# Performance work log

Hardware: AMD Instinct MI355X
Metric: run time of the kernel (lower is better)

The kernel has to match this reference:

```python
import jax, jax.numpy as jnp
import numpy as np

USER_NUM = 1_000_000
ITEM_NUM = 100_000
N_FEATS = 8
DICT_SIZE = 10_000
VEC_DIM = 16
K = 32
BATCH = 16_384
TOTAL_DIM = (2 + N_FEATS) * VEC_DIM  # 160


def setup_inputs() -> dict:
    key = jax.random.key(0)
    ks = jax.random.split(key, 7)
    inputs = jax.random.randint(ks[0], (BATCH, 2 + N_FEATS), 0, DICT_SIZE, dtype=jnp.int32)
    user_table = jax.random.normal(ks[1], (USER_NUM, VEC_DIM), dtype=jnp.float32) * 0.05
    item_table = jax.random.normal(ks[2], (ITEM_NUM, VEC_DIM), dtype=jnp.float32) * 0.05
    feat_tables = jax.random.normal(ks[3], (N_FEATS, DICT_SIZE, VEC_DIM), dtype=jnp.float32) * 0.05
    w = jax.random.normal(ks[4], (TOTAL_DIM, 1), dtype=jnp.float32) * 0.05
    b = jnp.zeros((1,), dtype=jnp.float32)
    k_mat = jax.random.normal(ks[5], (TOTAL_DIM, K), dtype=jnp.float32) * (1.0 / np.sqrt(TOTAL_DIM))
    return {"inputs": inputs, "user_table": user_table, "item_table": item_table,
            "feat_tables": feat_tables, "w": w, "b": b, "k_mat": k_mat}


def reference(inputs, user_table, item_table, feat_tables, w, b, k_mat):
    B = inputs.shape[0]
    user_vec = user_table[inputs[:, 0]]            # [B, D]
    item_vec = item_table[inputs[:, 1]]            # [B, D]
    # gather each feature table with its own id column: [F, B, D]
    feat_vecs = jax.vmap(lambda tbl, idx: tbl[idx], in_axes=(0, 1))(feat_tables, inputs[:, 2:])
    feat_flat = jnp.transpose(feat_vecs, (1, 0, 2)).reshape(B, -1)  # [B, F*D]
    x = jnp.concatenate([user_vec, item_vec, feat_flat], axis=1)    # [B, total_dim]
    linear = x @ w + b                                              # [B, 1]
    inter_1 = jnp.square(x @ k_mat)                                 # [B, K]
    inter_2 = jnp.square(x) @ jnp.square(k_mat)                     # [B, K]
    cross = 0.5 * jnp.sum(inter_1 - inter_2, axis=1, keepdims=True) # [B, 1]
    return jax.nn.sigmoid(linear + cross)
```

## Files before the change

kernel.cpp:

```cpp
#include <hip/hip_runtime.h>
#include <hip/hip_bf16.h>
#include <math.h>

#define NFEAT 10
#define DICT 10000

typedef __attribute__((ext_vector_type(8))) short bf16x8;
typedef __attribute__((ext_vector_type(4))) float f32x4;
typedef __attribute__((ext_vector_type(4))) unsigned u32x4;

__device__ inline unsigned short f2bf(float f) {
    __hip_bfloat16 h = __float2bfloat16(f);
    unsigned short s;
    __builtin_memcpy(&s, &h, sizeof(s));
    return s;
}
__device__ inline unsigned cvt2(float lo, float hi) {
    return (unsigned)f2bf(lo) | ((unsigned)f2bf(hi) << 16);
}

__global__ __launch_bounds__(256, 2) void fm_fused(
    const int* __restrict__ inputs,
    const float* __restrict__ user_table,
    const float* __restrict__ item_table,
    const float* __restrict__ feat_tables,
    const float* __restrict__ wvec,
    const float* __restrict__ bb,
    const float* __restrict__ k_mat,
    float* __restrict__ out)
{
    __shared__ float part_t[2][16];

    const int tid   = threadIdx.x;
    const int lane  = tid & 63;
    const int wid   = tid >> 6;
    const int tile  = wid >> 1;
    const bool sq   = (wid & 1) != 0;
    const int gtile = blockIdx.x * 2 + tile;
    const int col   = lane & 15;
    const int kg    = lane >> 4;
    const int e     = gtile * 16 + col;
    const int fsel  = kg >> 1;
    const int hoff  = (kg & 1) * 8;

    int idx[5];
    #pragma unroll
    for (int c = 0; c < 5; ++c)
        idx[c] = inputs[e * NFEAT + 2 * c + fsel];

    float4 u0[5], u1[5];
    #pragma unroll
    for (int c = 0; c < 5; ++c) {
        const float* tbl = (c == 0)
            ? (fsel ? item_table : user_table)
            : (feat_tables + (size_t)(2 * c + fsel - 2) * (DICT * 16));
        const float* src = tbl + (size_t)idx[c] * 16 + hoff;
        u0[c] = *(const float4*)src;
        u1[c] = *(const float4*)(src + 4);
    }

    bf16x8 b0[5], b1[5];
    #pragma unroll
    for (int c = 0; c < 5; ++c) {
        const int dbase = c * 32 + kg * 8;
        float f0[8], f1[8];
        #pragma unroll
        for (int j = 0; j < 8; ++j) {
            f0[j] = k_mat[(dbase + j) * 32 + col];
            f1[j] = k_mat[(dbase + j) * 32 + 16 + col];
        }
        if (sq) {
            #pragma unroll
            for (int j = 0; j < 8; ++j) { f0[j] *= f0[j]; f1[j] *= f1[j]; }
        }
        u32x4 p0, p1;
        #pragma unroll
        for (int j = 0; j < 4; ++j) {
            p0[j] = cvt2(f0[2*j], f0[2*j+1]);
            p1[j] = cvt2(f1[2*j], f1[2*j+1]);
        }
        b0[c] = __builtin_bit_cast(bf16x8, p0);
        b1[c] = __builtin_bit_cast(bf16x8, p1);
    }

    f32x4 acc0 = {0,0,0,0};
    f32x4 acc1 = {0,0,0,0};
    #pragma unroll
    for (int c = 0; c < 5; ++c) {
        float4 v0 = u0[c], v1 = u1[c];
        if (sq) {
            v0.x *= v0.x; v0.y *= v0.y; v0.z *= v0.z; v0.w *= v0.w;
            v1.x *= v1.x; v1.y *= v1.y; v1.z *= v1.z; v1.w *= v1.w;
        }
        u32x4 p;
        p[0] = cvt2(v0.x, v0.y); p[1] = cvt2(v0.z, v0.w);
        p[2] = cvt2(v1.x, v1.y); p[3] = cvt2(v1.z, v1.w);
        bf16x8 a = __builtin_bit_cast(bf16x8, p);
        acc0 = __builtin_amdgcn_mfma_f32_16x16x32_bf16(a, b0[c], acc0, 0, 0, 0);
        acc1 = __builtin_amdgcn_mfma_f32_16x16x32_bf16(a, b1[c], acc1, 0, 0, 0);
    }

    float lin = 0.f;
    if (!sq) {
        #pragma unroll
        for (int c = 0; c < 5; ++c) {
            const int dbase = c * 32 + kg * 8;
            float4 w0 = *(const float4*)&wvec[dbase];
            float4 w1 = *(const float4*)&wvec[dbase + 4];
            lin = fmaf(u0[c].x, w0.x, lin); lin = fmaf(u0[c].y, w0.y, lin);
            lin = fmaf(u0[c].z, w0.z, lin); lin = fmaf(u0[c].w, w0.w, lin);
            lin = fmaf(u1[c].x, w1.x, lin); lin = fmaf(u1[c].y, w1.y, lin);
            lin = fmaf(u1[c].z, w1.z, lin); lin = fmaf(u1[c].w, w1.w, lin);
        }
        lin += __shfl_xor(lin, 16, 64);
        lin += __shfl_xor(lin, 32, 64);
    }

    float sv[4];
    #pragma unroll
    for (int r = 0; r < 4; ++r) {
        float v = sq ? (acc0[r] + acc1[r])
                     : (acc0[r]*acc0[r] + acc1[r]*acc1[r]);
        #pragma unroll
        for (int m = 1; m <= 8; m <<= 1)
            v += __shfl_xor(v, m, 64);
        sv[r] = v;
        if (sq && col == 0) part_t[tile][kg * 4 + r] = v;
    }
    __syncthreads();

    if (!sq) {
        const float bval = bb[0];
        #pragma unroll
        for (int r = 0; r < 4; ++r) {
            float lm = __shfl(lin, kg * 4 + r, 64);
            if (col == 0) {
                float z = lm + bval + 0.5f * (sv[r] - part_t[tile][kg * 4 + r]);
                out[gtile * 16 + kg * 4 + r] = 1.0f / (1.0f + __expf(-z));
            }
        }
    }
}

extern "C" void kernel_launch(void* const* d_in, const int* in_sizes, int n_in,
                              void* d_out, int out_size, void* d_ws, size_t ws_size,
                              hipStream_t stream) {
    const int*   inputs      = (const int*)  d_in[0];
    const float* user_table  = (const float*)d_in[1];
    const float* item_table  = (const float*)d_in[2];
    const float* feat_tables = (const float*)d_in[3];
    const float* w           = (const float*)d_in[4];
    const float* b           = (const float*)d_in[5];
    const float* k_mat       = (const float*)d_in[6];
    float* out = (float*)d_out;

    int nblocks = out_size / 32;
    fm_fused<<<nblocks, 256, 0, stream>>>(inputs, user_table, item_table,
                                          feat_tables, w, b, k_mat, out);
}
```

Baseline: 11.81 us.

## Split K columns across waves so each block handles one 16-row tile

Each block now processes a single 16-sample tile with four waves: two compute the x·K halves (16 columns each) and two compute the squared halves. The linear term is done by wave 0 only, and partial sums are combined through shared memory. This halves per-wave MFMA and k_mat load work, doubles the grid size, and raises the launch-bounds occupancy hint. In exchange, every wave now re-gathers the same embedding rows, so redundant table loads per sample double.

```diff
diff --git a/kernel.cpp b/kernel.cpp
--- a/kernel.cpp
+++ b/kernel.cpp
@@ -19,7 +19,7 @@
     return (unsigned)f2bf(lo) | ((unsigned)f2bf(hi) << 16);
 }
 
-__global__ __launch_bounds__(256, 2) void fm_fused(
+__global__ __launch_bounds__(256, 4) void fm_fused(
     const int* __restrict__ inputs,
     const float* __restrict__ user_table,
     const float* __restrict__ item_table,
@@ -29,19 +29,19 @@
     const float* __restrict__ k_mat,
     float* __restrict__ out)
 {
-    __shared__ float part_t[2][16];
+    __shared__ float part[5][16];
 
     const int tid   = threadIdx.x;
     const int lane  = tid & 63;
     const int wid   = tid >> 6;
-    const int tile  = wid >> 1;
-    const bool sq   = (wid & 1) != 0;
-    const int gtile = blockIdx.x * 2 + tile;
+    const int gtile = blockIdx.x;
     const int col   = lane & 15;
     const int kg    = lane >> 4;
     const int e     = gtile * 16 + col;
     const int fsel  = kg >> 1;
     const int hoff  = (kg & 1) * 8;
+    const int kh    = (wid & 1) * 16;
+    const bool sq   = (wid >= 2);
 
     int idx[5];
     #pragma unroll
@@ -59,32 +59,26 @@
         u1[c] = *(const float4*)(src + 4);
     }
 
-    bf16x8 b0[5], b1[5];
+    bf16x8 bf[5];
     #pragma unroll
     for (int c = 0; c < 5; ++c) {
         const int dbase = c * 32 + kg * 8;
-        float f0[8], f1[8];
+        float f[8];
         #pragma unroll
-        for (int j = 0; j < 8; ++j) {
-            f0[j] = k_mat[(dbase + j) * 32 + col];
-            f1[j] = k_mat[(dbase + j) * 32 + 16 + col];
-        }
+        for (int j = 0; j < 8; ++j)
+            f[j] = k_mat[(dbase + j) * 32 + kh + col];
         if (sq) {
             #pragma unroll
-            for (int j = 0; j < 8; ++j) { f0[j] *= f0[j]; f1[j] *= f1[j]; }
+            for (int j = 0; j < 8; ++j) f[j] *= f[j];
         }
-        u32x4 p0, p1;
+        u32x4 p;
         #pragma unroll
-        for (int j = 0; j < 4; ++j) {
-            p0[j] = cvt2(f0[2*j], f0[2*j+1]);
-            p1[j] = cvt2(f1[2*j], f1[2*j+1]);
-        }
-        b0[c] = __builtin_bit_cast(bf16x8, p0);
-        b1[c] = __builtin_bit_cast(bf16x8, p1);
+        for (int j = 0; j < 4; ++j)
+            p[j] = cvt2(f[2*j], f[2*j+1]);
+        bf[c] = __builtin_bit_cast(bf16x8, p);
     }
 
-    f32x4 acc0 = {0,0,0,0};
-    f32x4 acc1 = {0,0,0,0};
+    f32x4 acc = {0, 0, 0, 0};
     #pragma unroll
     for (int c = 0; c < 5; ++c) {
         float4 v0 = u0[c], v1 = u1[c];
@@ -96,12 +90,11 @@
         p[0] = cvt2(v0.x, v0.y); p[1] = cvt2(v0.z, v0.w);
         p[2] = cvt2(v1.x, v1.y); p[3] = cvt2(v1.z, v1.w);
         bf16x8 a = __builtin_bit_cast(bf16x8, p);
-        acc0 = __builtin_amdgcn_mfma_f32_16x16x32_bf16(a, b0[c], acc0, 0, 0, 0);
-        acc1 = __builtin_amdgcn_mfma_f32_16x16x32_bf16(a, b1[c], acc1, 0, 0, 0);
+        acc = __builtin_amdgcn_mfma_f32_16x16x32_bf16(a, bf[c], acc, 0, 0, 0);
     }
 
-    float lin = 0.f;
-    if (!sq) {
+    if (wid == 0) {
+        float lin = 0.f;
         #pragma unroll
         for (int c = 0; c < 5; ++c) {
             const int dbase = c * 32 + kg * 8;
@@ -114,31 +107,24 @@
         }
         lin += __shfl_xor(lin, 16, 64);
         lin += __shfl_xor(lin, 32, 64);
+        if (lane < 16) part[4][lane] = lin;
     }
 
-    float sv[4];
     #pragma unroll
     for (int r = 0; r < 4; ++r) {
-        float v = sq ? (acc0[r] + acc1[r])
-                     : (acc0[r]*acc0[r] + acc1[r]*acc1[r]);
+        float v = sq ? acc[r] : acc[r] * acc[r];
         #pragma unroll
         for (int m = 1; m <= 8; m <<= 1)
             v += __shfl_xor(v, m, 64);
-        sv[r] = v;
-        if (sq && col == 0) part_t[tile][kg * 4 + r] = v;
+        if (col == 0) part[wid][kg * 4 + r] = v;
     }
     __syncthreads();
 
-    if (!sq) {
-        const float bval = bb[0];
-        #pragma unroll
-        for (int r = 0; r < 4; ++r) {
-            float lm = __shfl(lin, kg * 4 + r, 64);
-            if (col == 0) {
-                float z = lm + bval + 0.5f * (sv[r] - part_t[tile][kg * 4 + r]);
-                out[gtile * 16 + kg * 4 + r] = 1.0f / (1.0f + __expf(-z));
-            }
-        }
+    if (tid < 16) {
+        float s2 = part[0][tid] + part[1][tid];
+        float t  = part[2][tid] + part[3][tid];
+        float z  = part[4][tid] + bb[0] + 0.5f * (s2 - t);
+        out[gtile * 16 + tid] = 1.0f / (1.0f + __expf(-z));
     }
 }
 
@@ -154,7 +140,7 @@
     const float* k_mat       = (const float*)d_in[6];
     float* out = (float*)d_out;
 
-    int nblocks = out_size / 32;
+    int nblocks = out_size / 16;
     fm_fused<<<nblocks, 256, 0, stream>>>(inputs, user_table, item_table,
                                           feat_tables, w, b, k_mat, out);
 }
```

After: 12.83 us. 1.09x slower.
